# Kernel optimization log

Hardware: AMD Instinct MI355X
Metric: run time of the kernel (lower is better)

Reference implementation:

```python
import jax, jax.numpy as jnp
import numpy as np

C = 256
HEADS = 8
HEAD_DIM = C // HEADS
GROUPS = 8
EPS = 1e-5


def setup_inputs() -> dict:
    key = jax.random.key(0)
    ks = jax.random.split(key, 11)
    B, S = 2, 16
    s = 0.02
    return {
        "x": jax.random.normal(ks[0], (B, C, S, S, S), dtype=jnp.float32),
        "gn_w": jnp.ones((C,), jnp.float32),
        "gn_b": jnp.zeros((C,), jnp.float32),
        "wq": jax.random.normal(ks[1], (C, C), jnp.float32) * s,
        "bq": jnp.zeros((C,), jnp.float32),
        "wk": jax.random.normal(ks[2], (C, C), jnp.float32) * s,
        "bk": jnp.zeros((C,), jnp.float32),
        "wv": jax.random.normal(ks[3], (C, C), jnp.float32) * s,
        "bv": jnp.zeros((C,), jnp.float32),
        "wo": jax.random.normal(ks[4], (C, C), jnp.float32) * s,
        "bo": jnp.zeros((C,), jnp.float32),
    }


def _group_norm(x, w, b):
    # x: [B, C, D, H, W]; GroupNorm(8, C) with affine params
    B, Cc, D, H, W = x.shape
    xg = x.reshape(B, GROUPS, Cc // GROUPS, D, H, W)
    mu = jnp.mean(xg, axis=(2, 3, 4, 5), keepdims=True)
    var = jnp.mean(jnp.square(xg - mu), axis=(2, 3, 4, 5), keepdims=True)
    xn = ((xg - mu) * jax.lax.rsqrt(var + EPS)).reshape(B, Cc, D, H, W)
    return xn * w[None, :, None, None, None] + b[None, :, None, None, None]


def reference(x, gn_w, gn_b, wq, bq, wk, bk, wv, bv, wo, bo):
    B, Cc, D, H, W = x.shape
    N = D * H * W
    xn = _group_norm(x, gn_w, gn_b).reshape(B, Cc, N)  # [B,C,N]
    # 1x1x1 Conv3d == per-voxel linear: weight [out,in]
    Q = jnp.einsum("oc,bcn->bon", wq, xn) + bq[None, :, None]
    K = jnp.einsum("oc,bcn->bon", wk, xn) + bk[None, :, None]
    V = jnp.einsum("oc,bcn->bon", wv, xn) + bv[None, :, None]
    Q = Q.reshape(B, HEADS, HEAD_DIM, N)
    K = K.reshape(B, HEADS, HEAD_DIM, N)
    V = V.reshape(B, HEADS, HEAD_DIM, N)
    scale = np.sqrt(HEAD_DIM).astype(np.float32)
    attn = jnp.einsum("bhdn,bhdm->bhnm", Q, K) / scale
    attn = jax.nn.softmax(attn, axis=-1)
    out = jnp.einsum("bhnm,bhdm->bhdn", attn, V)  # [B,h,hd,N]
    out = out.reshape(B, Cc, N)
    out = jnp.einsum("oc,bcn->bon", wo, out) + bo[None, :, None]
    return x + out.reshape(B, Cc, D, H, W)
```

## Files before the change

### kernel.cpp

```cpp
#include <hip/hip_runtime.h>

#define B_   2
#define C_   256
#define N_   4096
#define H_   8
#define HD_  32
#define G_   8
#define CPG_ 32

typedef short short8 __attribute__((ext_vector_type(8)));
typedef short short4v __attribute__((ext_vector_type(4)));
typedef unsigned uint4v __attribute__((ext_vector_type(4)));
typedef float f32x4  __attribute__((ext_vector_type(4)));
typedef float f4     __attribute__((ext_vector_type(4)));

__device__ __forceinline__ float b2f(short s) {
    return __uint_as_float(((unsigned)(unsigned short)s) << 16);
}
__device__ __forceinline__ short f2b(float f) {
    unsigned u = __float_as_uint(f);
    unsigned r = (u + 0x7FFF + ((u >> 16) & 1)) >> 16;
    return (short)r;
}

__global__ __launch_bounds__(256) void gn_part(const float* __restrict__ x,
                                               float* __restrict__ part) {
    int blk = blockIdx.x;
    const f4* p = (const f4*)x + (size_t)(blk >> 6) * (CPG_ * N_ / 4) + (size_t)(blk & 63) * 512;
    float s = 0.f, ss = 0.f;
#pragma unroll
    for (int i = 0; i < 2; i++) {
        f4 v = p[threadIdx.x + i * 256];
#pragma unroll
        for (int j = 0; j < 4; j++) { float f = v[j]; s += f; ss += f * f; }
    }
#pragma unroll
    for (int off = 32; off > 0; off >>= 1) {
        s  += __shfl_down(s, off);
        ss += __shfl_down(ss, off);
    }
    __shared__ float rs[4], rss[4];
    int w = threadIdx.x >> 6;
    if ((threadIdx.x & 63) == 0) { rs[w] = s; rss[w] = ss; }
    __syncthreads();
    if (threadIdx.x == 0) {
        part[blk * 2]     = rs[0] + rs[1] + rs[2] + rs[3];
        part[blk * 2 + 1] = rss[0] + rss[1] + rss[2] + rss[3];
    }
}

__global__ __launch_bounds__(256) void gemm_qkv(
    const float* __restrict__ x,
    const float* __restrict__ gw, const float* __restrict__ gb,
    const float* __restrict__ part,
    const float* __restrict__ wq, const float* __restrict__ bq,
    const float* __restrict__ wk, const float* __restrict__ bk,
    const float* __restrict__ wv, const float* __restrict__ bv,
    short* __restrict__ q, short* __restrict__ kt, short* __restrict__ v) {
    int z = blockIdx.z;
    int b = z / 3, which = z % 3;
    const float* W    = which == 0 ? wq : (which == 1 ? wk : wv);
    const float* bias = which == 0 ? bq : (which == 1 ? bk : bv);
    bool trans = (which != 2);
    float mul = (which == 0) ? (0.17677669529663687f * 1.4426950408889634f) : 1.0f;

    __shared__ short wl[64][40];
    __shared__ short xl[128][40];
    __shared__ float ga[256], gbb[256];
    __shared__ float mus[8], rstds[8];

    int o0 = blockIdx.y * 64, n0 = blockIdx.x * 128;
    int tid = threadIdx.x;
    int w = tid >> 6, lane = tid & 63, li = lane & 15, quad = lane >> 4;
    int wr = w & 1, wc = w >> 1;

#pragma unroll
    for (int gi = 0; gi < 2; gi++) {
        int g = w * 2 + gi;
        const float* pp = &part[(size_t)(b * 8 + g) * 128 + lane * 2];
        float s = pp[0], ss = pp[1];
#pragma unroll
        for (int off = 32; off > 0; off >>= 1) {
            s  += __shfl_down(s, off);
            ss += __shfl_down(ss, off);
        }
        if (lane == 0) {
            const float inv = 1.f / (float)(CPG_ * N_);
            float mu = s * inv;
            float var = ss * inv - mu * mu;
            mus[g] = mu;
            rstds[g] = rsqrtf(var + 1e-5f);
        }
    }
    __syncthreads();
    {
        int c = tid, g = c >> 5;
        float a = rstds[g] * gw[c];
        ga[c]  = a;
        gbb[c] = gb[c] - mus[g] * a;
    }

    f32x4 acc[8];
#pragma unroll
    for (int i = 0; i < 8; i++) acc[i] = (f32x4){0.f, 0.f, 0.f, 0.f};

    int cpair = tid >> 4, l16 = tid & 15;
    __syncthreads();

    for (int k0 = 0; k0 < 256; k0 += 32) {
        {
            int row = tid >> 2, co = (tid & 3) << 3;
            const float* wp = &W[(size_t)(o0 + row) * 256 + k0 + co];
            f4 wa = *(const f4*)wp;
            f4 wb = *(const f4*)(wp + 4);
            short8 w8;
#pragma unroll
            for (int j = 0; j < 4; j++) { w8[j] = f2b(wa[j]); w8[j + 4] = f2b(wb[j]); }
            *(short8*)&wl[row][co] = w8;
        }
        {
            int c0 = k0 + cpair * 2;
            float a0 = ga[c0],     b0c = gbb[c0];
            float a1 = ga[c0 + 1], b1c = gbb[c0 + 1];
            const float* xr0 = x + ((size_t)(b * 256 + c0)) * N_ + n0 + l16;
            const float* xr1 = xr0 + N_;
#pragma unroll
            for (int j = 0; j < 8; j++) {
                unsigned lo = (unsigned short)f2b(xr0[16 * j] * a0 + b0c);
                unsigned hi = (unsigned short)f2b(xr1[16 * j] * a1 + b1c);
                *(unsigned*)&xl[l16 + 16 * j][cpair * 2] = lo | (hi << 16);
            }
        }
        __syncthreads();
        short8 af[4], bfr[4];
        if (trans) {
#pragma unroll
            for (int i = 0; i < 4; i++) af[i]  = *(short8*)&xl[wr * 64 + i * 16 + li][quad * 8];
#pragma unroll
            for (int j = 0; j < 2; j++) bfr[j] = *(short8*)&wl[wc * 32 + j * 16 + li][quad * 8];
#pragma unroll
            for (int i = 0; i < 4; i++)
#pragma unroll
                for (int j = 0; j < 2; j++)
                    acc[i * 2 + j] = __builtin_amdgcn_mfma_f32_16x16x32_bf16(af[i], bfr[j], acc[i * 2 + j], 0, 0, 0);
        } else {
#pragma unroll
            for (int i = 0; i < 2; i++) af[i]  = *(short8*)&wl[wr * 32 + i * 16 + li][quad * 8];
#pragma unroll
            for (int j = 0; j < 4; j++) bfr[j] = *(short8*)&xl[wc * 64 + j * 16 + li][quad * 8];
#pragma unroll
            for (int i = 0; i < 2; i++)
#pragma unroll
                for (int j = 0; j < 4; j++)
                    acc[i * 4 + j] = __builtin_amdgcn_mfma_f32_16x16x32_bf16(af[i], bfr[j], acc[i * 4 + j], 0, 0, 0);
        }
        __syncthreads();
    }

    if (which == 2) {
        short* outp = v + (size_t)b * C_ * N_;
#pragma unroll
        for (int i = 0; i < 2; i++) {
            int ob = o0 + wr * 32 + i * 16 + quad * 4;
#pragma unroll
            for (int j = 0; j < 4; j++) {
                int n_ = n0 + wc * 64 + j * 16 + li;
#pragma unroll
                for (int r = 0; r < 4; r++) {
                    float val = acc[i * 4 + j][r] + bias[ob + r];
                    outp[(size_t)(ob + r) * N_ + n_] = f2b(val);
                }
            }
        }
    } else if (which == 0) {
        short* outp = q + (size_t)b * N_ * C_;
#pragma unroll
        for (int i = 0; i < 4; i++) {
            int nb_ = n0 + wr * 64 + i * 16 + quad * 4;
#pragma unroll
            for (int j = 0; j < 2; j++) {
                int o_ = o0 + wc * 32 + j * 16 + li;
                float bv_ = bias[o_];
#pragma unroll
                for (int r = 0; r < 4; r++)
                    outp[(size_t)(nb_ + r) * C_ + o_] = f2b((acc[i * 2 + j][r] + bv_) * mul);
            }
        }
    } else {
#pragma unroll
        for (int i = 0; i < 4; i++) {
            int nb_ = n0 + wr * 64 + i * 16 + quad * 4;
#pragma unroll
            for (int j = 0; j < 2; j++) {
                int o_ = o0 + wc * 32 + j * 16 + li;
                int hh = o_ >> 5, d = o_ & 31;
                float bv_ = bias[o_];
                short* kdst = kt + ((size_t)(b * 8 + hh) * N_) * HD_ + d;
#pragma unroll
                for (int r = 0; r < 4; r++)
                    kdst[(size_t)(nb_ + r) * HD_] = f2b(acc[i * 2 + j][r] + bv_);
            }
        }
    }
}

__global__ __launch_bounds__(512) void flash(const short* __restrict__ q,
                                             const short* __restrict__ ktp,
                                             const short* __restrict__ v,
                                             short* __restrict__ aoT) {
    int bid = blockIdx.x;
    int xcd = bid & 7;
    int rest = bid >> 3;
    int bh = xcd * 2 + (rest & 1);
    int nb = rest >> 1;
    int b = bh >> 3, h = bh & 7;

    const short* QT = q   + (size_t)b * N_ * C_ + h * HD_;
    const short* KP = ktp + (size_t)bh * N_ * HD_;
    const short* V  = v   + ((size_t)b * C_ + h * HD_) * N_;
    short* O = aoT + (size_t)b * N_ * C_ + h * HD_;

    __shared__ short kl[2 * 2560];
    __shared__ short vl[2 * 2304];

    int tid = threadIdx.x, w = tid >> 6, lane = tid & 63, li = lane & 15, quad = lane >> 4;
    int n0w = nb * 256 + w * 32;

    short8 qf0 = *(const short8*)&QT[(size_t)(n0w + li) * 256 + quad * 8];
    short8 qf1 = *(const short8*)&QT[(size_t)(n0w + 16 + li) * 256 + quad * 8];

    f32x4 oa00 = (f32x4){0.f,0.f,0.f,0.f}, oa01 = oa00, oa10 = oa00, oa11 = oa00;
    float lr0 = 0.f, lr1 = 0.f;
    const f32x4 zero = (f32x4){0.f, 0.f, 0.f, 0.f};

    int krow = tid >> 3, kcol = (tid & 7) << 2;
    const short* kgp = KP + (size_t)krow * HD_ + kcol;
    int klo = krow * 40 + kcol;
    int vd = tid >> 4, g = tid & 15;
    int mbase = 32 * (g >> 3) + 16 * (g & 1) + 4 * ((g >> 1) & 3);
    const short* vgp = V + (size_t)vd * N_ + mbase;
    int vlo = vd * 72 + g * 4;

    short4v kst = *(const short4v*)kgp;
    short4v vst = *(const short4v*)vgp;

    f32x4 s0[4], s1[4];
    short8 vf[4];

    for (int t = 0; t < 64; ++t) {
        int buf = t & 1;
        *(short4v*)&kl[buf * 2560 + klo] = kst;
        *(short4v*)&vl[buf * 2304 + vlo] = vst;
        if (t < 63) {
            kst = *(const short4v*)(kgp + (size_t)(t + 1) * 64 * HD_);
            vst = *(const short4v*)(vgp + (t + 1) * 64);
        }
        __syncthreads();

        __builtin_amdgcn_s_setprio(1);
#pragma unroll
        for (int c = 0; c < 4; c++) {
            short8 kf = *(short8*)&kl[buf * 2560 + (c * 16 + li) * 40 + quad * 8];
            s0[c] = __builtin_amdgcn_mfma_f32_16x16x32_bf16(kf, qf0, zero, 0, 0, 0);
            s1[c] = __builtin_amdgcn_mfma_f32_16x16x32_bf16(kf, qf1, zero, 0, 0, 0);
        }
        __builtin_amdgcn_s_setprio(0);

        vf[0] = *(short8*)&vl[buf * 2304 + li * 72 + quad * 8];
        vf[1] = *(short8*)&vl[buf * 2304 + (16 + li) * 72 + quad * 8];
        vf[2] = *(short8*)&vl[buf * 2304 + li * 72 + 32 + quad * 8];
        vf[3] = *(short8*)&vl[buf * 2304 + (16 + li) * 72 + 32 + quad * 8];

        unsigned paw[8];
        float lp = 0.f;
#pragma unroll
        for (int c = 0; c < 4; c++) {
            float e0 = __builtin_amdgcn_exp2f(s0[c][0]);
            float e1 = __builtin_amdgcn_exp2f(s0[c][1]);
            float e2 = __builtin_amdgcn_exp2f(s0[c][2]);
            float e3 = __builtin_amdgcn_exp2f(s0[c][3]);
            lp += (e0 + e1) + (e2 + e3);
            paw[2 * c]     = __builtin_amdgcn_perm(__float_as_uint(e1), __float_as_uint(e0), 0x07060302);
            paw[2 * c + 1] = __builtin_amdgcn_perm(__float_as_uint(e3), __float_as_uint(e2), 0x07060302);
        }
        lr0 += lp;
        uint4v p0 = (uint4v){paw[0], paw[1], paw[2], paw[3]};
        uint4v p1 = (uint4v){paw[4], paw[5], paw[6], paw[7]};
        short8 a0 = __builtin_bit_cast(short8, p0);
        short8 a1 = __builtin_bit_cast(short8, p1);

        lp = 0.f;
#pragma unroll
        for (int c = 0; c < 4; c++) {
            float e0 = __builtin_amdgcn_exp2f(s1[c][0]);
            float e1 = __builtin_amdgcn_exp2f(s1[c][1]);
            float e2 = __builtin_amdgcn_exp2f(s1[c][2]);
            float e3 = __builtin_amdgcn_exp2f(s1[c][3]);
            lp += (e0 + e1) + (e2 + e3);
            paw[2 * c]     = __builtin_amdgcn_perm(__float_as_uint(e1), __float_as_uint(e0), 0x07060302);
            paw[2 * c + 1] = __builtin_amdgcn_perm(__float_as_uint(e3), __float_as_uint(e2), 0x07060302);
        }
        lr1 += lp;
        uint4v p2 = (uint4v){paw[0], paw[1], paw[2], paw[3]};
        uint4v p3 = (uint4v){paw[4], paw[5], paw[6], paw[7]};
        short8 a2 = __builtin_bit_cast(short8, p2);
        short8 a3 = __builtin_bit_cast(short8, p3);

        __builtin_amdgcn_s_setprio(1);
        oa00 = __builtin_amdgcn_mfma_f32_16x16x32_bf16(a0, vf[0], oa00, 0, 0, 0);
        oa01 = __builtin_amdgcn_mfma_f32_16x16x32_bf16(a0, vf[1], oa01, 0, 0, 0);
        oa00 = __builtin_amdgcn_mfma_f32_16x16x32_bf16(a1, vf[2], oa00, 0, 0, 0);
        oa01 = __builtin_amdgcn_mfma_f32_16x16x32_bf16(a1, vf[3], oa01, 0, 0, 0);
        oa10 = __builtin_amdgcn_mfma_f32_16x16x32_bf16(a2, vf[0], oa10, 0, 0, 0);
        oa11 = __builtin_amdgcn_mfma_f32_16x16x32_bf16(a2, vf[1], oa11, 0, 0, 0);
        oa10 = __builtin_amdgcn_mfma_f32_16x16x32_bf16(a3, vf[2], oa10, 0, 0, 0);
        oa11 = __builtin_amdgcn_mfma_f32_16x16x32_bf16(a3, vf[3], oa11, 0, 0, 0);
        __builtin_amdgcn_s_setprio(0);
    }

    lr0 += __shfl_xor(lr0, 16); lr0 += __shfl_xor(lr0, 32);
    lr1 += __shfl_xor(lr1, 16); lr1 += __shfl_xor(lr1, 32);
#pragma unroll
    for (int r = 0; r < 4; r++) {
        float ln0 = __shfl(lr0, quad * 4 + r);
        float inv0 = 1.f / ln0;
        size_t n_ = (size_t)(n0w + quad * 4 + r);
        O[n_ * 256 + li]      = f2b(oa00[r] * inv0);
        O[n_ * 256 + 16 + li] = f2b(oa01[r] * inv0);
        float ln1 = __shfl(lr1, quad * 4 + r);
        float inv1 = 1.f / ln1;
        size_t n2 = (size_t)(n0w + 16 + quad * 4 + r);
        O[n2 * 256 + li]      = f2b(oa10[r] * inv1);
        O[n2 * 256 + 16 + li] = f2b(oa11[r] * inv1);
    }
}

__global__ __launch_bounds__(256) void gemm_out(const float* __restrict__ W,
                                                const float* __restrict__ bias,
                                                const short* __restrict__ aoT,
                                                const float* __restrict__ resid,
                                                float* __restrict__ out) {
    int b = blockIdx.z;
    const short* X = aoT + (size_t)b * N_ * C_;
    const float* R = resid + (size_t)b * C_ * N_;
    float* outp = out + (size_t)b * C_ * N_;

    __shared__ short wl[64][40];
    __shared__ short xl[64][40];

    int o0 = blockIdx.y * 64, n0 = blockIdx.x * 64;
    int tid = threadIdx.x;
    int w = tid >> 6, lane = tid & 63, li = lane & 15, quad = lane >> 4;
    int wr = w & 1, wc = w >> 1;

    f32x4 acc[2][2];
#pragma unroll
    for (int i = 0; i < 2; i++)
#pragma unroll
        for (int j = 0; j < 2; j++) acc[i][j] = (f32x4){0.f, 0.f, 0.f, 0.f};

    int row = tid >> 2, co = (tid & 3) << 3;
    for (int k0 = 0; k0 < 256; k0 += 32) {
        {
            const float* wp = &W[(size_t)(o0 + row) * 256 + k0 + co];
            f4 wa = *(const f4*)wp;
            f4 wb = *(const f4*)(wp + 4);
            short8 w8;
#pragma unroll
            for (int j = 0; j < 4; j++) { w8[j] = f2b(wa[j]); w8[j + 4] = f2b(wb[j]); }
            *(short8*)&wl[row][co] = w8;
        }
        *(short8*)&xl[row][co] = *(const short8*)&X[(size_t)(n0 + row) * 256 + k0 + co];
        __syncthreads();
        short8 af[2], bfr[2];
#pragma unroll
        for (int i = 0; i < 2; i++) af[i]  = *(short8*)&wl[wr * 32 + i * 16 + li][quad * 8];
#pragma unroll
        for (int j = 0; j < 2; j++) bfr[j] = *(short8*)&xl[wc * 32 + j * 16 + li][quad * 8];
#pragma unroll
        for (int i = 0; i < 2; i++)
#pragma unroll
            for (int j = 0; j < 2; j++)
                acc[i][j] = __builtin_amdgcn_mfma_f32_16x16x32_bf16(af[i], bfr[j], acc[i][j], 0, 0, 0);
        __syncthreads();
    }
#pragma unroll
    for (int i = 0; i < 2; i++) {
        int ob = o0 + wr * 32 + i * 16 + quad * 4;
#pragma unroll
        for (int j = 0; j < 2; j++) {
            int n_ = n0 + wc * 32 + j * 16 + li;
#pragma unroll
            for (int r = 0; r < 4; r++) {
                size_t idx = (size_t)(ob + r) * N_ + n_;
                outp[idx] = acc[i][j][r] + bias[ob + r] + R[idx];
            }
        }
    }
}

extern "C" void kernel_launch(void* const* d_in, const int* in_sizes, int n_in,
                              void* d_out, int out_size, void* d_ws, size_t ws_size,
                              hipStream_t stream) {
    const float* x  = (const float*)d_in[0];
    const float* gw = (const float*)d_in[1];
    const float* gb = (const float*)d_in[2];
    const float* wq = (const float*)d_in[3];
    const float* bq = (const float*)d_in[4];
    const float* wk = (const float*)d_in[5];
    const float* bk = (const float*)d_in[6];
    const float* wv = (const float*)d_in[7];
    const float* bv = (const float*)d_in[8];
    const float* wo = (const float*)d_in[9];
    const float* bo = (const float*)d_in[10];
    float* out = (float*)d_out;

    char* ws = (char*)d_ws;
    float* part = (float*)ws;
    const size_t TS = (size_t)B_ * N_ * C_;
    short* aoT = (short*)(ws + 16384);
    short* q   = aoT + TS;
    short* kt  = q + TS;
    short* v   = kt + TS;

    gn_part<<<1024, 256, 0, stream>>>(x, part);
    gemm_qkv<<<dim3(32, 4, 6), 256, 0, stream>>>(x, gw, gb, part,
                                                 wq, bq, wk, bk, wv, bv, q, kt, v);
    flash<<<256, 512, 0, stream>>>(q, kt, v, aoT);
    gemm_out<<<dim3(64, 4, 2), 256, 0, stream>>>(wo, bo, aoT, x, out);
}
```

Before: 150.0 us.

## Fuse Q/K/V projections into one block and pre-convert weights to bf16

```diff
diff --git a/kernel.cpp b/kernel.cpp
--- a/kernel.cpp
+++ b/kernel.cpp
@@ -49,27 +49,40 @@
     }
 }
 
-__global__ __launch_bounds__(256) void gemm_qkv(
+__global__ __launch_bounds__(256) void wconv(const float* __restrict__ wq,
+                                             const float* __restrict__ wk,
+                                             const float* __restrict__ wv,
+                                             const float* __restrict__ wo,
+                                             short* __restrict__ wb) {
+    int gid = blockIdx.x * 256 + threadIdx.x;
+    int rid = gid >> 13;
+    int off = (gid & 8191) * 8;
+    const float* src = rid == 0 ? wq : (rid == 1 ? wk : (rid == 2 ? wv : wo));
+    f4 a = *(const f4*)(src + off);
+    f4 b = *(const f4*)(src + off + 4);
+    short8 r;
+#pragma unroll
+    for (int j = 0; j < 4; j++) { r[j] = f2b(a[j]); r[j + 4] = f2b(b[j]); }
+    *(short8*)&wb[(size_t)rid * 65536 + off] = r;
+}
+
+__global__ __launch_bounds__(256, 2) void gemm_qkv(
     const float* __restrict__ x,
     const float* __restrict__ gw, const float* __restrict__ gb,
     const float* __restrict__ part,
-    const float* __restrict__ wq, const float* __restrict__ bq,
-    const float* __restrict__ wk, const float* __restrict__ bk,
-    const float* __restrict__ wv, const float* __restrict__ bv,
+    const short* __restrict__ wb,
+    const float* __restrict__ bq, const float* __restrict__ bk,
+    const float* __restrict__ bv,
     short* __restrict__ q, short* __restrict__ kt, short* __restrict__ v) {
-    int z = blockIdx.z;
-    int b = z / 3, which = z % 3;
-    const float* W    = which == 0 ? wq : (which == 1 ? wk : wv);
-    const float* bias = which == 0 ? bq : (which == 1 ? bk : bv);
-    bool trans = (which != 2);
-    float mul = (which == 0) ? (0.17677669529663687f * 1.4426950408889634f) : 1.0f;
-
-    __shared__ short wl[64][40];
-    __shared__ short xl[128][40];
+    int b = blockIdx.z;
+    int o0 = blockIdx.y * 64, n0 = blockIdx.x * 64;
+    const float mul = 0.17677669529663687f * 1.4426950408889634f;
+
+    __shared__ short wl[3][64][40];
+    __shared__ short xl[64][40];
     __shared__ float ga[256], gbb[256];
     __shared__ float mus[8], rstds[8];
 
-    int o0 = blockIdx.y * 64, n0 = blockIdx.x * 128;
     int tid = threadIdx.x;
     int w = tid >> 6, lane = tid & 63, li = lane & 15, quad = lane >> 4;
     int wr = w & 1, wc = w >> 1;
@@ -100,24 +113,25 @@
         gbb[c] = gb[c] - mus[g] * a;
     }
 
-    f32x4 acc[8];
-#pragma unroll
-    for (int i = 0; i < 8; i++) acc[i] = (f32x4){0.f, 0.f, 0.f, 0.f};
-
+    f32x4 aq[2][2], ak[2][2], av[2][2];
+#pragma unroll
+    for (int i = 0; i < 2; i++)
+#pragma unroll
+        for (int j = 0; j < 2; j++) {
+            aq[i][j] = (f32x4){0.f, 0.f, 0.f, 0.f};
+            ak[i][j] = (f32x4){0.f, 0.f, 0.f, 0.f};
+            av[i][j] = (f32x4){0.f, 0.f, 0.f, 0.f};
+        }
+
+    int wrow = tid >> 2, wco = (tid & 3) << 3;
     int cpair = tid >> 4, l16 = tid & 15;
     __syncthreads();
 
     for (int k0 = 0; k0 < 256; k0 += 32) {
-        {
-            int row = tid >> 2, co = (tid & 3) << 3;
-            const float* wp = &W[(size_t)(o0 + row) * 256 + k0 + co];
-            f4 wa = *(const f4*)wp;
-            f4 wb = *(const f4*)(wp + 4);
-            short8 w8;
-#pragma unroll
-            for (int j = 0; j < 4; j++) { w8[j] = f2b(wa[j]); w8[j + 4] = f2b(wb[j]); }
-            *(short8*)&wl[row][co] = w8;
-        }
+#pragma unroll
+        for (int m = 0; m < 3; m++)
+            *(short8*)&wl[m][wrow][wco] =
+                *(const short8*)&wb[(size_t)m * 65536 + (size_t)(o0 + wrow) * 256 + k0 + wco];
         {
             int c0 = k0 + cpair * 2;
             float a0 = ga[c0],     b0c = gbb[c0];
@@ -125,80 +139,75 @@
             const float* xr0 = x + ((size_t)(b * 256 + c0)) * N_ + n0 + l16;
             const float* xr1 = xr0 + N_;
 #pragma unroll
-            for (int j = 0; j < 8; j++) {
+            for (int j = 0; j < 4; j++) {
                 unsigned lo = (unsigned short)f2b(xr0[16 * j] * a0 + b0c);
                 unsigned hi = (unsigned short)f2b(xr1[16 * j] * a1 + b1c);
                 *(unsigned*)&xl[l16 + 16 * j][cpair * 2] = lo | (hi << 16);
             }
         }
         __syncthreads();
-        short8 af[4], bfr[4];
-        if (trans) {
-#pragma unroll
-            for (int i = 0; i < 4; i++) af[i]  = *(short8*)&xl[wr * 64 + i * 16 + li][quad * 8];
-#pragma unroll
-            for (int j = 0; j < 2; j++) bfr[j] = *(short8*)&wl[wc * 32 + j * 16 + li][quad * 8];
-#pragma unroll
-            for (int i = 0; i < 4; i++)
-#pragma unroll
-                for (int j = 0; j < 2; j++)
-                    acc[i * 2 + j] = __builtin_amdgcn_mfma_f32_16x16x32_bf16(af[i], bfr[j], acc[i * 2 + j], 0, 0, 0);
-        } else {
-#pragma unroll
-            for (int i = 0; i < 2; i++) af[i]  = *(short8*)&wl[wr * 32 + i * 16 + li][quad * 8];
-#pragma unroll
-            for (int j = 0; j < 4; j++) bfr[j] = *(short8*)&xl[wc * 64 + j * 16 + li][quad * 8];
-#pragma unroll
-            for (int i = 0; i < 2; i++)
-#pragma unroll
-                for (int j = 0; j < 4; j++)
-                    acc[i * 4 + j] = __builtin_amdgcn_mfma_f32_16x16x32_bf16(af[i], bfr[j], acc[i * 4 + j], 0, 0, 0);
+
+        short8 xf[2];
+#pragma unroll
+        for (int i = 0; i < 2; i++)
+            xf[i] = *(short8*)&xl[wc * 32 + i * 16 + li][quad * 8];
+#pragma unroll
+        for (int j = 0; j < 2; j++) {
+            short8 wfq = *(short8*)&wl[0][wr * 32 + j * 16 + li][quad * 8];
+            short8 wfk = *(short8*)&wl[1][wr * 32 + j * 16 + li][quad * 8];
+            short8 wfv = *(short8*)&wl[2][wr * 32 + j * 16 + li][quad * 8];
+#pragma unroll
+            for (int i = 0; i < 2; i++) {
+                aq[i][j] = __builtin_amdgcn_mfma_f32_16x16x32_bf16(xf[i], wfq, aq[i][j], 0, 0, 0);
+                ak[i][j] = __builtin_amdgcn_mfma_f32_16x16x32_bf16(xf[i], wfk, ak[i][j], 0, 0, 0);
+                av[j][i] = __builtin_amdgcn_mfma_f32_16x16x32_bf16(wfv, xf[i], av[j][i], 0, 0, 0);
+            }
         }
         __syncthreads();
     }
 
-    if (which == 2) {
+    {
+        short* outp = q + (size_t)b * N_ * C_;
+#pragma unroll
+        for (int i = 0; i < 2; i++) {
+            int nb_ = n0 + wc * 32 + i * 16 + quad * 4;
+#pragma unroll
+            for (int j = 0; j < 2; j++) {
+                int o_ = o0 + wr * 32 + j * 16 + li;
+                float bv_ = bq[o_];
+#pragma unroll
+                for (int r = 0; r < 4; r++)
+                    outp[(size_t)(nb_ + r) * C_ + o_] = f2b((aq[i][j][r] + bv_) * mul);
+            }
+        }
+    }
+    {
+#pragma unroll
+        for (int i = 0; i < 2; i++) {
+            int nb_ = n0 + wc * 32 + i * 16 + quad * 4;
+#pragma unroll
+            for (int j = 0; j < 2; j++) {
+                int o_ = o0 + wr * 32 + j * 16 + li;
+                int hh = o_ >> 5, d = o_ & 31;
+                float bv_ = bk[o_];
+                short* kdst = kt + ((size_t)(b * 8 + hh) * N_) * HD_ + d;
+#pragma unroll
+                for (int r = 0; r < 4; r++)
+                    kdst[(size_t)(nb_ + r) * HD_] = f2b(ak[i][j][r] + bv_);
+            }
+        }
+    }
+    {
         short* outp = v + (size_t)b * C_ * N_;
 #pragma unroll
-        for (int i = 0; i < 2; i++) {
-            int ob = o0 + wr * 32 + i * 16 + quad * 4;
-#pragma unroll
-            for (int j = 0; j < 4; j++) {
-                int n_ = n0 + wc * 64 + j * 16 + li;
-#pragma unroll
-                for (int r = 0; r < 4; r++) {
-                    float val = acc[i * 4 + j][r] + bias[ob + r];
-                    outp[(size_t)(ob + r) * N_ + n_] = f2b(val);
-                }
-            }
-        }
-    } else if (which == 0) {
-        short* outp = q + (size_t)b * N_ * C_;
-#pragma unroll
-        for (int i = 0; i < 4; i++) {
-            int nb_ = n0 + wr * 64 + i * 16 + quad * 4;
-#pragma unroll
-            for (int j = 0; j < 2; j++) {
-                int o_ = o0 + wc * 32 + j * 16 + li;
-                float bv_ = bias[o_];
+        for (int j = 0; j < 2; j++) {
+            int ob = o0 + wr * 32 + j * 16 + quad * 4;
+#pragma unroll
+            for (int i = 0; i < 2; i++) {
+                int n_ = n0 + wc * 32 + i * 16 + li;
 #pragma unroll
                 for (int r = 0; r < 4; r++)
-                    outp[(size_t)(nb_ + r) * C_ + o_] = f2b((acc[i * 2 + j][r] + bv_) * mul);
-            }
-        }
-    } else {
-#pragma unroll
-        for (int i = 0; i < 4; i++) {
-            int nb_ = n0 + wr * 64 + i * 16 + quad * 4;
-#pragma unroll
-            for (int j = 0; j < 2; j++) {
-                int o_ = o0 + wc * 32 + j * 16 + li;
-                int hh = o_ >> 5, d = o_ & 31;
-                float bv_ = bias[o_];
-                short* kdst = kt + ((size_t)(b * 8 + hh) * N_) * HD_ + d;
-#pragma unroll
-                for (int r = 0; r < 4; r++)
-                    kdst[(size_t)(nb_ + r) * HD_] = f2b(acc[i * 2 + j][r] + bv_);
+                    outp[(size_t)(ob + r) * N_ + n_] = f2b(av[j][i][r] + bv[ob + r]);
             }
         }
     }
@@ -335,7 +344,7 @@
     }
 }
 
-__global__ __launch_bounds__(256) void gemm_out(const float* __restrict__ W,
+__global__ __launch_bounds__(256) void gemm_out(const short* __restrict__ wob,
                                                 const float* __restrict__ bias,
                                                 const short* __restrict__ aoT,
                                                 const float* __restrict__ resid,
@@ -361,15 +370,7 @@
 
     int row = tid >> 2, co = (tid & 3) << 3;
     for (int k0 = 0; k0 < 256; k0 += 32) {
-        {
-            const float* wp = &W[(size_t)(o0 + row) * 256 + k0 + co];
-            f4 wa = *(const f4*)wp;
-            f4 wb = *(const f4*)(wp + 4);
-            short8 w8;
-#pragma unroll
-            for (int j = 0; j < 4; j++) { w8[j] = f2b(wa[j]); w8[j + 4] = f2b(wb[j]); }
-            *(short8*)&wl[row][co] = w8;
-        }
+        *(short8*)&wl[row][co] = *(const short8*)&wob[(size_t)(o0 + row) * 256 + k0 + co];
         *(short8*)&xl[row][co] = *(const short8*)&X[(size_t)(n0 + row) * 256 + k0 + co];
         __syncthreads();
         short8 af[2], bfr[2];
@@ -422,10 +423,12 @@
     short* q   = aoT + TS;
     short* kt  = q + TS;
     short* v   = kt + TS;
+    short* wb  = v + TS;
 
     gn_part<<<1024, 256, 0, stream>>>(x, part);
-    gemm_qkv<<<dim3(32, 4, 6), 256, 0, stream>>>(x, gw, gb, part,
-                                                 wq, bq, wk, bk, wv, bv, q, kt, v);
+    wconv<<<128, 256, 0, stream>>>(wq, wk, wv, wo, wb);
+    gemm_qkv<<<dim3(64, 4, 2), 256, 0, stream>>>(x, gw, gb, part, wb,
+                                                 bq, bk, bv, q, kt, v);
     flash<<<256, 512, 0, stream>>>(q, kt, v, aoT);
-    gemm_out<<<dim3(64, 4, 2), 256, 0, stream>>>(wo, bo, aoT, x, out);
-}
+    gemm_out<<<dim3(64, 4, 2), 256, 0, stream>>>(wb + 3 * 65536, bo, aoT, x, out);
+}
```

Result: no change. 147.7 us (-1.5%).
